# Kernel optimization log

Hardware: AMD Instinct MI355X
Metric: run time of the kernel (lower is better)

Reference implementation:

```python
import jax, jax.numpy as jnp
import numpy as np

NQ = 8    # QCNN qubits
NLQ = 4   # QLSTM qubits == hidden_dim
C64 = jnp.complex64

H_GATE = (1.0 / np.sqrt(2.0)) * jnp.array([[1, 1], [1, -1]], dtype=C64)


def ap1(st, U, q):
    # apply 2x2 gate U on qubit axis q of state st (shape (2,)*n)
    s = jnp.moveaxis(st, q, -1)
    s = jnp.einsum('ij,...j->...i', U, s)
    return jnp.moveaxis(s, -1, q)


def apcx(st, c, t):
    # CNOT with control c, target t: flip target slice where control == 1
    s = jnp.moveaxis(st, (c, t), (-2, -1))
    s = jnp.stack([s[..., 0, :], s[..., 1, ::-1]], axis=-2)
    return jnp.moveaxis(s, (-2, -1), (c, t))


def RX(t):
    c = jnp.cos(t / 2).astype(C64)
    s = (-1j * jnp.sin(t / 2)).astype(C64)
    return jnp.stack([jnp.stack([c, s]), jnp.stack([s, c])])


def RY(t):
    c = jnp.cos(t / 2)
    s = jnp.sin(t / 2)
    return jnp.stack([jnp.stack([c, -s]), jnp.stack([s, c])]).astype(C64)


def RZ(t):
    e = jnp.exp(-0.5j * t).astype(C64)
    z = jnp.zeros((), C64)
    return jnp.stack([jnp.stack([e, z]), jnp.stack([z, jnp.conj(e)])])


def PH(t):
    # qiskit phase gate P(t) = diag(1, e^{i t})
    e = jnp.exp(1j * t).astype(C64)
    o = jnp.ones((), C64)
    z = jnp.zeros((), C64)
    return jnp.stack([jnp.stack([o, z]), jnp.stack([z, e])])


def init_state(n):
    st = jnp.zeros((2,) * n, C64)
    return st.at[(0,) * n].set(1.0)


def zexp(st, q):
    # <Z_q> of statevector st
    p = st.real ** 2 + st.imag ** 2
    m = p.sum(axis=tuple(a for a in range(st.ndim) if a != q))
    return m[0] - m[1]


def conv_block(st, p, q1, q2):
    st = ap1(st, RZ(-np.pi / 2), q2)
    st = apcx(st, q2, q1)
    st = ap1(st, RZ(p[0]), q1)
    st = ap1(st, RY(p[1]), q2)
    st = apcx(st, q1, q2)
    st = ap1(st, RY(p[2]), q2)
    st = apcx(st, q2, q1)
    st = ap1(st, RZ(np.pi / 2), q1)
    return st


def pool_block(st, p, src, sink):
    st = ap1(st, RZ(-np.pi / 2), sink)
    st = apcx(st, sink, src)
    st = ap1(st, RZ(p[0]), src)
    st = ap1(st, RY(p[1]), sink)
    st = apcx(st, src, sink)
    st = ap1(st, RY(p[2]), sink)
    return st


QCNN_SPECS = [
    (conv_block, [(0, 1), (2, 3), (4, 5), (6, 7)]),  # c1
    (pool_block, [(0, 1), (2, 3), (4, 5), (6, 7)]),  # p1
    (conv_block, [(0, 1), (2, 3)]),                  # c2
    (pool_block, [(0, 1), (2, 3)]),                  # p2
    (conv_block, [(0, 1)]),                          # c3
    (pool_block, [(0, 1)]),                          # p3
]


def qcnn_single(x, w):
    # x: (8,) feature angles, w: (42,) ansatz weights
    st = init_state(NQ)
    for _ in range(2):
        for q in range(NQ):
            st = ap1(st, H_GATE, q)
        for q in range(NQ):
            st = ap1(st, PH(2.0 * x[q]), q)
    idx = 0
    for blk, prs in QCNN_SPECS:
        for a, b in prs:
            st = blk(st, w[idx:idx + 3], a, b)
            idx += 3
    return zexp(st, NQ - 1)  # 'ZIIIIIII' => Z on qubit 7 (little-endian)


def qgate_single(v, theta):
    # v: (4,) encoder angles (per sample), theta: (4,) trainable RX angles
    st = init_state(NLQ)
    for i in range(NLQ):
        st = ap1(st, RX(v[i]), i)
    for i in range(NLQ):
        st = ap1(st, RX(theta[i]), i)
    for i in range(NLQ - 1):
        st = apcx(st, i, i + 1)
    st = apcx(st, NLQ - 1, 0)
    return jnp.stack([zexp(st, q) for q in range(NLQ)])


qgate = jax.vmap(qgate_single, in_axes=(0, None))


def setup_inputs() -> dict:
    key = jax.random.key(0)
    ks = jax.random.split(key, 12)
    B, S = 16, 128
    x = jax.random.uniform(ks[0], (B, S, NQ), jnp.float32) * np.pi
    qcnn_w = jax.random.normal(ks[1], (42,), jnp.float32) * 0.1

    def lin(k, out_d, in_d):
        k1, k2 = jax.random.split(k)
        lim = 1.0 / np.sqrt(in_d)
        W = jax.random.uniform(k1, (out_d, in_d), jnp.float32, -lim, lim)
        b = jax.random.uniform(k2, (out_d,), jnp.float32, -lim, lim)
        return W, b

    Wf, bf = lin(ks[2], NLQ, 1 + NLQ)
    Wi, bi = lin(ks[3], NLQ, 1 + NLQ)
    Wg, bg = lin(ks[4], NLQ, 1 + NLQ)
    Wo, bo = lin(ks[5], NLQ, 1 + NLQ)
    theta_f = jax.random.normal(ks[6], (NLQ,), jnp.float32) * 0.1
    theta_i = jax.random.normal(ks[7], (NLQ,), jnp.float32) * 0.1
    theta_g = jax.random.normal(ks[8], (NLQ,), jnp.float32) * 0.1
    theta_o = jax.random.normal(ks[9], (NLQ,), jnp.float32) * 0.1
    Wh, bh = lin(ks[10], 1, NLQ)
    return dict(x=x, qcnn_w=qcnn_w, theta_f=theta_f, theta_i=theta_i,
                theta_g=theta_g, theta_o=theta_o, Wf=Wf, bf=bf, Wi=Wi, bi=bi,
                Wg=Wg, bg=bg, Wo=Wo, bo=bo, Wh=Wh, bh=bh)


def reference(x, qcnn_w, theta_f, theta_i, theta_g, theta_o,
              Wf, bf, Wi, bi, Wg, bg, Wo, bo, Wh, bh):
    B, S, _ = x.shape
    flat = x.reshape(B * S, NQ)
    qcnn_out = jax.vmap(qcnn_single, in_axes=(0, None))(flat, qcnn_w)
    qcnn_out = qcnn_out.reshape(B, S, 1)
    lstm_in = jnp.transpose(qcnn_out, (1, 0, 2))  # (S, B, 1)
    h0 = jnp.zeros((B, NLQ), x.dtype)
    c0 = jnp.zeros((B, NLQ), x.dtype)

    def step(carry, xt):
        hx, cx = carry
        comb = jnp.concatenate([xt, hx], axis=1)  # (B, 1 + hidden)
        f = jax.nn.sigmoid(qgate(comb @ Wf.T + bf, theta_f))
        i = jax.nn.sigmoid(qgate(comb @ Wi.T + bi, theta_i))
        g = jnp.tanh(qgate(comb @ Wg.T + bg, theta_g))
        o = jax.nn.sigmoid(qgate(comb @ Wo.T + bo, theta_o))
        cx = f * cx + i * g
        hx = o * jnp.tanh(cx)
        return (hx, cx), hx

    _, outs = jax.lax.scan(step, (h0, c0), lstm_in)  # outs: (S, B, hidden)
    logits = outs[-1] @ Wh.T + bh  # (B, 1)
    return qcnn_out, logits
```

## Files before the change

### kernel.cpp

```cpp
#include <hip/hip_runtime.h>
#include <math.h>

#define PI_F 3.14159265358979323846f
#define FLAG_MAGIC 0x9E3779B9u

typedef int v2i __attribute__((ext_vector_type(2)));

__device__ __forceinline__ float rcpf(float x) { return __builtin_amdgcn_rcpf(x); }
__device__ __forceinline__ void fswap(float2& p, float2& q) { float2 t = p; p = q; q = t; }


template<int Q>
__device__ __forceinline__ float exq(float v) {
    if constexpr (Q == 2)
        return __int_as_float(__builtin_amdgcn_update_dpp(0, __float_as_int(v), 0xB1, 0xF, 0xF, true));
    else if constexpr (Q == 3)
        return __int_as_float(__builtin_amdgcn_update_dpp(0, __float_as_int(v), 0x4E, 0xF, 0xF, true));
    else if constexpr (Q == 4)
        return __int_as_float(__builtin_amdgcn_ds_swizzle(__float_as_int(v), 0x101F));
    else if constexpr (Q == 5)
        return __int_as_float(__builtin_amdgcn_ds_swizzle(__float_as_int(v), 0x201F));
    else if constexpr (Q == 6)
        return __int_as_float(__builtin_amdgcn_ds_swizzle(__float_as_int(v), 0x401F));
    else {
        v2i r = __builtin_amdgcn_permlane32_swap(__float_as_int(v), __float_as_int(v), false, false);
        return __int_as_float((threadIdx.x & 32) ? r[0] : r[1]);
    }
}

template<int Q>
__device__ __forceinline__ void rzg(float2 a[4], float th, int lane) {
    float c = __cosf(0.5f * th), s = __sinf(0.5f * th);
    if constexpr (Q >= 2) {
        float se = ((lane >> (Q - 2)) & 1) ? s : -s;
        #pragma unroll
        for (int r = 0; r < 4; ++r) {
            float nx = c * a[r].x - se * a[r].y;
            float ny = c * a[r].y + se * a[r].x;
            a[r] = make_float2(nx, ny);
        }
    } else {
        #pragma unroll
        for (int r = 0; r < 4; ++r) {
            int bit = (Q == 0) ? (r >> 1) : (r & 1);
            float se = bit ? s : -s;
            float nx = c * a[r].x - se * a[r].y;
            float ny = c * a[r].y + se * a[r].x;
            a[r] = make_float2(nx, ny);
        }
    }
}

template<int Q>
__device__ __forceinline__ void ryg(float2 a[4], float th, int lane) {
    float c = __cosf(0.5f * th), s = __sinf(0.5f * th);
    if constexpr (Q >= 2) {
        float se = ((lane >> (Q - 2)) & 1) ? s : -s;
        #pragma unroll
        for (int r = 0; r < 4; ++r) {
            float ox = exq<Q>(a[r].x), oy = exq<Q>(a[r].y);
            a[r] = make_float2(c * a[r].x + se * ox, c * a[r].y + se * oy);
        }
    } else if constexpr (Q == 0) {
        #pragma unroll
        for (int r = 0; r < 2; ++r) {
            float2 lo = a[r], hi = a[r + 2];
            a[r]     = make_float2(c * lo.x - s * hi.x, c * lo.y - s * hi.y);
            a[r + 2] = make_float2(s * lo.x + c * hi.x, s * lo.y + c * hi.y);
        }
    } else {
        #pragma unroll
        for (int r = 0; r < 4; r += 2) {
            float2 lo = a[r], hi = a[r + 1];
            a[r]     = make_float2(c * lo.x - s * hi.x, c * lo.y - s * hi.y);
            a[r + 1] = make_float2(s * lo.x + c * hi.x, s * lo.y + c * hi.y);
        }
    }
}

template<int C, int T>
__device__ __forceinline__ void cxg(float2 a[4], int lane) {
    if constexpr (C >= 2) {
        bool cb = (lane >> (C - 2)) & 1;
        #pragma unroll
        for (int r = 0; r < 4; ++r) {
            float ox = exq<T>(a[r].x), oy = exq<T>(a[r].y);
            a[r].x = cb ? ox : a[r].x;
            a[r].y = cb ? oy : a[r].y;
        }
    } else if constexpr (C == 0 && T == 1) {
        fswap(a[2], a[3]);
    } else {
        fswap(a[1], a[3]);
    }
}

template<int Q>
__device__ __forceinline__ void featg(float2 a[4], float xq, int lane) {
    float phi = 2.0f * xq;
    float e1x = __cosf(phi), e1y = __sinf(phi);
    float e2x = e1x * e1x - e1y * e1y;
    float e2y = 2.0f * e1x * e1y;
    float2 u00 = make_float2(0.5f * (1.0f + e1x),  0.5f * e1y);
    float2 u01 = make_float2(0.5f * (1.0f - e1x), -0.5f * e1y);
    float2 u10 = make_float2(0.5f * (e1x - e2x), 0.5f * (e1y - e2y));
    float2 u11 = make_float2(0.5f * (e1x + e2x), 0.5f * (e1y + e2y));
    if constexpr (Q >= 2) {
        bool bset = (lane >> (Q - 2)) & 1;
        float csx = bset ? u11.x : u00.x, csy = bset ? u11.y : u00.y;
        float cox = bset ? u10.x : u01.x, coy = bset ? u10.y : u01.y;
        #pragma unroll
        for (int r = 0; r < 4; ++r) {
            float ox = exq<Q>(a[r].x), oy = exq<Q>(a[r].y);
            float nx = csx * a[r].x - csy * a[r].y + cox * ox - coy * oy;
            float ny = csx * a[r].y + csy * a[r].x + cox * oy + coy * ox;
            a[r] = make_float2(nx, ny);
        }
    } else {
        float2 l, h;
        #define APPL(LO, HI)                                                        \
            l = a[LO]; h = a[HI];                                                   \
            a[LO] = make_float2(u00.x*l.x - u00.y*l.y + u01.x*h.x - u01.y*h.y,      \
                                u00.x*l.y + u00.y*l.x + u01.x*h.y + u01.y*h.x);     \
            a[HI] = make_float2(u10.x*l.x - u10.y*l.y + u11.x*h.x - u11.y*h.y,      \
                                u10.x*l.y + u10.y*l.x + u11.x*h.y + u11.y*h.x);
        if constexpr (Q == 0) { APPL(0, 2) APPL(1, 3) }
        else                  { APPL(0, 1) APPL(2, 3) }
        #undef APPL
    }
}

template<int Q1, int Q2>
__device__ __forceinline__ void convg(float2 a[4], const float* __restrict__ p, int lane) {
    rzg<Q2>(a, -0.5f * PI_F, lane);
    cxg<Q2, Q1>(a, lane);
    rzg<Q1>(a, p[0], lane);
    ryg<Q2>(a, p[1], lane);
    cxg<Q1, Q2>(a, lane);
    ryg<Q2>(a, p[2], lane);
    cxg<Q2, Q1>(a, lane);
    rzg<Q1>(a, 0.5f * PI_F, lane);
}

template<int Q1, int Q2>
__device__ __forceinline__ void poolg(float2 a[4], const float* __restrict__ p, int lane) {
    rzg<Q2>(a, -0.5f * PI_F, lane);
    cxg<Q2, Q1>(a, lane);
    rzg<Q1>(a, p[0], lane);
    ryg<Q2>(a, p[1], lane);
    cxg<Q1, Q2>(a, lane);
    ryg<Q2>(a, p[2], lane);
}

template<int CTRL>
__device__ __forceinline__ float bq(float v) {
    return __int_as_float(__builtin_amdgcn_update_dpp(0, __float_as_int(v), CTRL, 0xF, 0xF, true));
}

__device__ __forceinline__ float pick4(bool b0, bool b1, float a0, float a1, float a2, float a3) {
    float t01 = b0 ? a1 : a0;
    float t23 = b0 ? a3 : a2;
    return b1 ? t23 : t01;
}


__device__ __forceinline__ void stage_chunk(int m, int lane, unsigned key,
                                            unsigned long long* __restrict__ flg,
                                            float* qsh) {
    int idx = m * 64 + lane;
    unsigned long long v = __hip_atomic_load(&flg[idx], __ATOMIC_RELAXED, __HIP_MEMORY_SCOPE_AGENT);
    while ((unsigned)v != key) {
        __builtin_amdgcn_s_sleep(1);
        v = __hip_atomic_load(&flg[idx], __ATOMIC_RELAXED, __HIP_MEMORY_SCOPE_AGENT);
    }
    qsh[(idx & 15) * 132 + (idx >> 4)] = __uint_as_float((unsigned)(v >> 32));
}

__global__ __launch_bounds__(256, 1) void fused_kernel(
    const float* __restrict__ x,  const float* __restrict__ w,
    const float* __restrict__ thf, const float* __restrict__ thi,
    const float* __restrict__ thg, const float* __restrict__ tho,
    const float* __restrict__ Wf, const float* __restrict__ bf,
    const float* __restrict__ Wi, const float* __restrict__ bi,
    const float* __restrict__ Wg, const float* __restrict__ bg,
    const float* __restrict__ Wo, const float* __restrict__ bo,
    const float* __restrict__ Wh, const float* __restrict__ bh,
    float* __restrict__ out, unsigned long long* __restrict__ flg) {
    __shared__ __align__(16) float qsh[16 * 132];
    int lane = threadIdx.x & 63;
    int wave = threadIdx.x >> 6;
    unsigned* epoch = (unsigned*)(flg + 2048);

    if (blockIdx.x != 512) {
        unsigned key = FLAG_MAGIC ^ __hip_atomic_load(epoch, __ATOMIC_RELAXED, __HIP_MEMORY_SCOPE_AGENT);
        int n = blockIdx.x * 4 + wave;
        int bb = n & 15, tt = n >> 4;
        int sidx = bb * 128 + tt;
        float2 a[4];
        a[0] = make_float2(lane == 0 ? 1.0f : 0.0f, 0.0f);
        a[1] = make_float2(0.0f, 0.0f);
        a[2] = make_float2(0.0f, 0.0f);
        a[3] = make_float2(0.0f, 0.0f);

        const float* xr = x + sidx * 8;
        featg<0>(a, xr[0], lane);
        featg<1>(a, xr[1], lane);
        featg<2>(a, xr[2], lane);
        featg<3>(a, xr[3], lane);
        featg<4>(a, xr[4], lane);
        featg<5>(a, xr[5], lane);
        featg<6>(a, xr[6], lane);
        featg<7>(a, xr[7], lane);

        convg<0,1>(a, w + 0,  lane);
        convg<2,3>(a, w + 3,  lane);
        convg<4,5>(a, w + 6,  lane);
        convg<6,7>(a, w + 9,  lane);
        poolg<0,1>(a, w + 12, lane);
        poolg<2,3>(a, w + 15, lane);
        poolg<4,5>(a, w + 18, lane);
        poolg<6,7>(a, w + 21, lane);
        convg<0,1>(a, w + 24, lane);
        convg<2,3>(a, w + 27, lane);
        poolg<0,1>(a, w + 30, lane);
        poolg<2,3>(a, w + 33, lane);
        convg<0,1>(a, w + 36, lane);
        poolg<0,1>(a, w + 39, lane);

        float ssum = 0.f;
        #pragma unroll
        for (int r = 0; r < 4; ++r)
            ssum += a[r].x * a[r].x + a[r].y * a[r].y;
        ssum = (lane & 32) ? -ssum : ssum;
        ssum += exq<2>(ssum);
        ssum += exq<3>(ssum);
        ssum += exq<4>(ssum);
        ssum += exq<5>(ssum);
        ssum += exq<6>(ssum);
        {
            v2i rr = __builtin_amdgcn_permlane32_swap(__float_as_int(ssum), __float_as_int(ssum), false, false);
            ssum = __int_as_float((threadIdx.x & 32) ? rr[0] : rr[1]) +
                   __int_as_float((threadIdx.x & 32) ? rr[1] : rr[0]);
        }
        if (lane == 0) {
            out[sidx] = ssum;
            unsigned long long pk = ((unsigned long long)__float_as_uint(ssum) << 32)
                                  | (unsigned long long)key;
            __hip_atomic_store(&flg[n], pk, __ATOMIC_RELAXED, __HIP_MEMORY_SCOPE_AGENT);
        }
        return;
    }

    if (wave != 0) return;
    unsigned key = FLAG_MAGIC ^ __hip_atomic_load(epoch, __ATOMIC_RELAXED, __HIP_MEMORY_SCOPE_AGENT);

    stage_chunk(0, lane, key, flg, qsh);
    __builtin_amdgcn_wave_barrier();

    int b = lane >> 2, q = lane & 3;
    bool qb0 = q & 1, qb1 = q & 2;
    const float* Wp = (q == 0) ? Wf : (q == 1) ? Wi : (q == 2) ? Wg : Wo;
    const float* bp = (q == 0) ? bf : (q == 1) ? bi : (q == 2) ? bg : bo;
    const float* tp = (q == 0) ? thf : (q == 1) ? thi : (q == 2) ? thg : tho;

    float W[20], av[4];
    #pragma unroll
    for (int k = 0; k < 20; ++k) W[k] = Wp[k];
    #pragma unroll
    for (int r = 0; r < 4; ++r) av[r] = bp[r] + tp[r];

    float nA = (q == 2) ? 1.0f : 0.0f;
    float nB = (q == 2) ? -2.0f : 1.0f;
    float nK = (q == 2) ? 2.0f : -1.0f;

    float c = 0.f;
    float h0 = 0.f, h1 = 0.f, h2 = 0.f, h3 = 0.f;
    const float* qrow = &qsh[b * 132];

    for (int j = 0; j < 32; ++j) {
        if (j < 31) stage_chunk(j + 1, lane, key, flg, qsh);
        __builtin_amdgcn_wave_barrier();
        #pragma unroll
        for (int k = 0; k < 4; ++k) {
            int t = 4 * j + k;
            float xv = qrow[t];
            float vA = av[0] + W[0]*xv  + W[1]*h0  + W[2]*h1  + W[3]*h2  + W[4]*h3;
            float vB = av[1] + W[5]*xv  + W[6]*h0  + W[7]*h1  + W[8]*h2  + W[9]*h3;
            float vC = av[2] + W[10]*xv + W[11]*h0 + W[12]*h1 + W[13]*h2 + W[14]*h3;
            float vD = av[3] + W[15]*xv + W[16]*h0 + W[17]*h1 + W[18]*h2 + W[19]*h3;
            float cA = __cosf(vA), cB = __cosf(vB), cC = __cosf(vC), cD = __cosf(vD);
            float r1 = cA * cB, r2 = r1 * cC, r3 = r2 * cD, r0 = cB * (cC * cD);
            float E0 = __expf(nK * r0), E1 = __expf(nK * r1);
            float E2 = __expf(nK * r2), E3 = __expf(nK * r3);
            float n0 = nA + nB * rcpf(E0 + 1.0f);
            float n1 = nA + nB * rcpf(E1 + 1.0f);
            float n2 = nA + nB * rcpf(E2 + 1.0f);
            float n3 = nA + nB * rcpf(E3 + 1.0f);
            float F0 = bq<0x00>(n0), F1 = bq<0x00>(n1), F2 = bq<0x00>(n2), F3 = bq<0x00>(n3);
            float I0 = bq<0x55>(n0), I1 = bq<0x55>(n1), I2 = bq<0x55>(n2), I3 = bq<0x55>(n3);
            float G0 = bq<0xAA>(n0), G1 = bq<0xAA>(n1), G2 = bq<0xAA>(n2), G3 = bq<0xAA>(n3);
            float O0 = bq<0xFF>(n0), O1 = bq<0xFF>(n1), O2 = bq<0xFF>(n2), O3 = bq<0xFF>(n3);
            float F = pick4(qb0, qb1, F0, F1, F2, F3);
            float I = pick4(qb0, qb1, I0, I1, I2, I3);
            float G = pick4(qb0, qb1, G0, G1, G2, G3);
            float O = pick4(qb0, qb1, O0, O1, O2, O3);
            c = F * c + I * G;
            float Ec = __expf(2.0f * c);
            float tau = 1.0f - 2.0f * rcpf(Ec + 1.0f);
            float hq = O * tau;
            h0 = bq<0x00>(hq);
            h1 = bq<0x55>(hq);
            h2 = bq<0xAA>(hq);
            h3 = bq<0xFF>(hq);
        }
    }

    if (q == 0)
        out[2048 + b] = bh[0] + Wh[0]*h0 + Wh[1]*h1 + Wh[2]*h2 + Wh[3]*h3;

    if (lane == 0)
        __hip_atomic_fetch_add(epoch, 1u, __ATOMIC_RELAXED, __HIP_MEMORY_SCOPE_AGENT);
}

extern "C" void kernel_launch(void* const* d_in, const int* in_sizes, int n_in,
                              void* d_out, int out_size, void* d_ws, size_t ws_size,
                              hipStream_t stream) {
    fused_kernel<<<513, 256, 0, stream>>>(
        (const float*)d_in[0],  (const float*)d_in[1],
        (const float*)d_in[2],  (const float*)d_in[3],
        (const float*)d_in[4],  (const float*)d_in[5],
        (const float*)d_in[6],  (const float*)d_in[7],
        (const float*)d_in[8],  (const float*)d_in[9],
        (const float*)d_in[10], (const float*)d_in[11],
        (const float*)d_in[12], (const float*)d_in[13],
        (const float*)d_in[14], (const float*)d_in[15],
        (float*)d_out, (unsigned long long*)d_ws);
}
```

Before: 122.6 us.

## Split LSTM recurrence across four waves with one gate element per lane

```diff
diff --git a/kernel.cpp b/kernel.cpp
--- a/kernel.cpp
+++ b/kernel.cpp
@@ -157,24 +157,11 @@
     return __int_as_float(__builtin_amdgcn_update_dpp(0, __float_as_int(v), CTRL, 0xF, 0xF, true));
 }
 
-__device__ __forceinline__ float pick4(bool b0, bool b1, float a0, float a1, float a2, float a3) {
-    float t01 = b0 ? a1 : a0;
-    float t23 = b0 ? a3 : a2;
-    return b1 ? t23 : t01;
-}
-
-
-__device__ __forceinline__ void stage_chunk(int m, int lane, unsigned key,
-                                            unsigned long long* __restrict__ flg,
-                                            float* qsh) {
-    int idx = m * 64 + lane;
-    unsigned long long v = __hip_atomic_load(&flg[idx], __ATOMIC_RELAXED, __HIP_MEMORY_SCOPE_AGENT);
-    while ((unsigned)v != key) {
-        __builtin_amdgcn_s_sleep(1);
-        v = __hip_atomic_load(&flg[idx], __ATOMIC_RELAXED, __HIP_MEMORY_SCOPE_AGENT);
-    }
-    qsh[(idx & 15) * 132 + (idx >> 4)] = __uint_as_float((unsigned)(v >> 32));
-}
+template<int OFF>
+__device__ __forceinline__ float swz(float v) {
+    return __int_as_float(__builtin_amdgcn_ds_swizzle(__float_as_int(v), OFF));
+}
+
 
 __global__ __launch_bounds__(256, 1) void fused_kernel(
     const float* __restrict__ x,  const float* __restrict__ w,
@@ -186,14 +173,14 @@
     const float* __restrict__ Wo, const float* __restrict__ bo,
     const float* __restrict__ Wh, const float* __restrict__ bh,
     float* __restrict__ out, unsigned long long* __restrict__ flg) {
-    __shared__ __align__(16) float qsh[16 * 132];
+    __shared__ __align__(16) float qsh[4][4 * 132];
     int lane = threadIdx.x & 63;
-    int wave = threadIdx.x >> 6;
+    int wv = threadIdx.x >> 6;
     unsigned* epoch = (unsigned*)(flg + 2048);
 
     if (blockIdx.x != 512) {
         unsigned key = FLAG_MAGIC ^ __hip_atomic_load(epoch, __ATOMIC_RELAXED, __HIP_MEMORY_SCOPE_AGENT);
-        int n = blockIdx.x * 4 + wave;
+        int n = blockIdx.x * 4 + wv;
         int bb = n & 15, tt = n >> 4;
         int sidx = bb * 128 + tt;
         float2 a[4];
@@ -251,59 +238,67 @@
         return;
     }
 
-    if (wave != 0) return;
     unsigned key = FLAG_MAGIC ^ __hip_atomic_load(epoch, __ATOMIC_RELAXED, __HIP_MEMORY_SCOPE_AGENT);
 
-    stage_chunk(0, lane, key, flg, qsh);
+    int j4 = lane & 3;
+    int g  = (lane >> 2) & 3;
+    int bl = (lane >> 4) & 3;
+    float* xrow = &qsh[wv][0];
+
+    const float* Wp = (g == 0) ? Wf : (g == 1) ? Wi : (g == 2) ? Wg : Wo;
+    const float* bp = (g == 0) ? bf : (g == 1) ? bi : (g == 2) ? bg : bo;
+    const float* tp = (g == 0) ? thf : (g == 1) ? thi : (g == 2) ? thg : tho;
+
+    float w0 = Wp[j4 * 5 + 0], w1 = Wp[j4 * 5 + 1], w2 = Wp[j4 * 5 + 2];
+    float w3 = Wp[j4 * 5 + 3], w4 = Wp[j4 * 5 + 4];
+    float av = bp[j4] + tp[j4];
+    float nA = (g == 2) ? 1.0f : 0.0f;
+    float nB = (g == 2) ? -2.0f : 1.0f;
+    float nK = (g == 2) ? 2.0f : -1.0f;
+
+    #define STAGE16(m)                                                              \
+        if (lane < 16) {                                                            \
+            int fidx = (4 * (m) + (lane >> 2)) * 16 + (wv * 4 + (lane & 3));        \
+            unsigned long long v = __hip_atomic_load(&flg[fidx], __ATOMIC_RELAXED,  \
+                                                     __HIP_MEMORY_SCOPE_AGENT);     \
+            while ((unsigned)v != key) {                                            \
+                __builtin_amdgcn_s_sleep(1);                                        \
+                v = __hip_atomic_load(&flg[fidx], __ATOMIC_RELAXED,                 \
+                                      __HIP_MEMORY_SCOPE_AGENT);                    \
+            }                                                                       \
+            xrow[(lane & 3) * 132 + 4 * (m) + (lane >> 2)] =                        \
+                __uint_as_float((unsigned)(v >> 32));                               \
+        }
+
+    STAGE16(0)
     __builtin_amdgcn_wave_barrier();
-
-    int b = lane >> 2, q = lane & 3;
-    bool qb0 = q & 1, qb1 = q & 2;
-    const float* Wp = (q == 0) ? Wf : (q == 1) ? Wi : (q == 2) ? Wg : Wo;
-    const float* bp = (q == 0) ? bf : (q == 1) ? bi : (q == 2) ? bg : bo;
-    const float* tp = (q == 0) ? thf : (q == 1) ? thi : (q == 2) ? thg : tho;
-
-    float W[20], av[4];
-    #pragma unroll
-    for (int k = 0; k < 20; ++k) W[k] = Wp[k];
-    #pragma unroll
-    for (int r = 0; r < 4; ++r) av[r] = bp[r] + tp[r];
-
-    float nA = (q == 2) ? 1.0f : 0.0f;
-    float nB = (q == 2) ? -2.0f : 1.0f;
-    float nK = (q == 2) ? 2.0f : -1.0f;
 
     float c = 0.f;
     float h0 = 0.f, h1 = 0.f, h2 = 0.f, h3 = 0.f;
-    const float* qrow = &qsh[b * 132];
 
     for (int j = 0; j < 32; ++j) {
-        if (j < 31) stage_chunk(j + 1, lane, key, flg, qsh);
+        if (j < 31) STAGE16(j + 1)
         __builtin_amdgcn_wave_barrier();
+        float4 xq4 = *(const float4*)&xrow[bl * 132 + 4 * j];
         #pragma unroll
         for (int k = 0; k < 4; ++k) {
-            int t = 4 * j + k;
-            float xv = qrow[t];
-            float vA = av[0] + W[0]*xv  + W[1]*h0  + W[2]*h1  + W[3]*h2  + W[4]*h3;
-            float vB = av[1] + W[5]*xv  + W[6]*h0  + W[7]*h1  + W[8]*h2  + W[9]*h3;
-            float vC = av[2] + W[10]*xv + W[11]*h0 + W[12]*h1 + W[13]*h2 + W[14]*h3;
-            float vD = av[3] + W[15]*xv + W[16]*h0 + W[17]*h1 + W[18]*h2 + W[19]*h3;
-            float cA = __cosf(vA), cB = __cosf(vB), cC = __cosf(vC), cD = __cosf(vD);
-            float r1 = cA * cB, r2 = r1 * cC, r3 = r2 * cD, r0 = cB * (cC * cD);
-            float E0 = __expf(nK * r0), E1 = __expf(nK * r1);
-            float E2 = __expf(nK * r2), E3 = __expf(nK * r3);
-            float n0 = nA + nB * rcpf(E0 + 1.0f);
-            float n1 = nA + nB * rcpf(E1 + 1.0f);
-            float n2 = nA + nB * rcpf(E2 + 1.0f);
-            float n3 = nA + nB * rcpf(E3 + 1.0f);
-            float F0 = bq<0x00>(n0), F1 = bq<0x00>(n1), F2 = bq<0x00>(n2), F3 = bq<0x00>(n3);
-            float I0 = bq<0x55>(n0), I1 = bq<0x55>(n1), I2 = bq<0x55>(n2), I3 = bq<0x55>(n3);
-            float G0 = bq<0xAA>(n0), G1 = bq<0xAA>(n1), G2 = bq<0xAA>(n2), G3 = bq<0xAA>(n3);
-            float O0 = bq<0xFF>(n0), O1 = bq<0xFF>(n1), O2 = bq<0xFF>(n2), O3 = bq<0xFF>(n3);
-            float F = pick4(qb0, qb1, F0, F1, F2, F3);
-            float I = pick4(qb0, qb1, I0, I1, I2, I3);
-            float G = pick4(qb0, qb1, G0, G1, G2, G3);
-            float O = pick4(qb0, qb1, O0, O1, O2, O3);
+            float xv = (k == 0) ? xq4.x : (k == 1) ? xq4.y : (k == 2) ? xq4.z : xq4.w;
+            float v = av + w0 * xv + w1 * h0 + w2 * h1 + w3 * h2 + w4 * h3;
+            float co = __cosf(v);
+            float b0 = bq<0x00>(co), b1 = bq<0x55>(co), b2 = bq<0xAA>(co), b3 = bq<0xFF>(co);
+            float p01 = b0 * b1;
+            float q23 = b2 * b3;
+            float a0  = b1 * q23;
+            float s   = (j4 == 1) ? 1.0f : b2;
+            float t   = p01 * s;
+            float t3  = t * b3;
+            float r   = (j4 == 0) ? a0 : ((j4 == 3) ? t3 : t);
+            float E = __expf(nK * r);
+            float n = nA + nB * rcpf(E + 1.0f);
+            float F = swz<0x013>(n);
+            float I = swz<0x093>(n);
+            float G = swz<0x113>(n);
+            float O = swz<0x193>(n);
             c = F * c + I * G;
             float Ec = __expf(2.0f * c);
             float tau = 1.0f - 2.0f * rcpf(Ec + 1.0f);
@@ -314,11 +309,12 @@
             h3 = bq<0xFF>(hq);
         }
     }
-
-    if (q == 0)
-        out[2048 + b] = bh[0] + Wh[0]*h0 + Wh[1]*h1 + Wh[2]*h2 + Wh[3]*h3;
-
-    if (lane == 0)
+    #undef STAGE16
+
+    if ((lane & 15) == 0)
+        out[2048 + wv * 4 + bl] = bh[0] + Wh[0]*h0 + Wh[1]*h1 + Wh[2]*h2 + Wh[3]*h3;
+
+    if (threadIdx.x == 0)
         __hip_atomic_fetch_add(epoch, 1u, __ATOMIC_RELAXED, __HIP_MEMORY_SCOPE_AGENT);
 }
 
```

Result: faster. 118.8 us (-3.1%).
